# Kernel tuning notes

Hardware: AMD Instinct MI355X
Metric: run time of the kernel (lower is better)

The kernel has to match this reference:

```python
import jax, jax.numpy as jnp
import numpy as np

N = 100000      # nodes
E = 3200000     # edges
F_IN = 512      # input features
H = 16          # hidden dim (as in source)
C = 7           # num classes (Cora)


def gcn_conv(x, W, b, src, dst, n):
    # GCNConv: linear transform, add self-loops, symmetric normalization,
    # scatter-add aggregation from src -> dst, then bias.
    h = x @ W                                   # [N, out]
    loop = jnp.arange(n)
    src_f = jnp.concatenate([src, loop])        # [E+N] with self-loops
    dst_f = jnp.concatenate([dst, loop])
    deg = jax.ops.segment_sum(jnp.ones_like(dst_f, dtype=h.dtype), dst_f, num_segments=n)
    dinv = jnp.where(deg > 0, jax.lax.rsqrt(deg), jnp.zeros_like(deg))
    norm = dinv[src_f] * dinv[dst_f]            # [E+N]
    msg = h[src_f] * norm[:, None]              # gather + scale
    out = jax.ops.segment_sum(msg, dst_f, num_segments=n)  # scatter-add
    return out + b


def setup_inputs() -> dict:
    key = jax.random.key(0)
    k1, k2, k3, k4 = jax.random.split(key, 4)
    x = jax.random.normal(k1, (N, F_IN), dtype=jnp.float32)
    edge_index = jax.random.randint(k2, (2, E), 0, N, dtype=jnp.int32)
    W1 = jax.random.normal(k3, (F_IN, H), dtype=jnp.float32) / np.sqrt(F_IN)
    b1 = jnp.zeros((H,), dtype=jnp.float32)
    W2 = jax.random.normal(k4, (H, C), dtype=jnp.float32) / np.sqrt(H)
    b2 = jnp.zeros((C,), dtype=jnp.float32)
    return {"x": x, "edge_index": edge_index, "W1": W1, "b1": b1, "W2": W2, "b2": b2}


def reference(x, edge_index, W1, b1, W2, b2):
    src, dst = edge_index[0], edge_index[1]
    h = gcn_conv(x, W1, b1, src, dst, N)
    h = jax.nn.relu(h)
    out = gcn_conv(h, W2, b2, src, dst, N)
    return jax.nn.log_softmax(out, axis=1)
```

## Files before the change

### kernel.cpp

```cpp
#include <hip/hip_runtime.h>
#include <math.h>

#define F_IN 512
#define HDIM 16
#define CDIM 7
#define NBLK 1024
#define BSH  9
#define BMASK ((1u << BSH) - 1u)

__global__ __launch_bounds__(256) void k_p2a(const int* __restrict__ dst,
                                             unsigned* __restrict__ hist_g,
                                             int E, int nbuck) {
    __shared__ unsigned lh[256];
    int blk = blockIdx.x;
    int t = threadIdx.x;
    lh[t] = 0u;
    __syncthreads();
    int per = (E + NBLK - 1) / NBLK;
    int s0 = blk * per;
    int e0 = min(E, s0 + per);
    for (int i = s0 + t; i < e0; i += 256)
        atomicAdd(&lh[((unsigned)dst[i]) >> BSH], 1u);
    __syncthreads();
    if (t < nbuck) hist_g[(size_t)t * NBLK + blk] = lh[t];
}

__global__ __launch_bounds__(256) void k_scan_buckets(unsigned* __restrict__ hist_g,
                                                      unsigned* __restrict__ count) {
    __shared__ unsigned s[256];
    int b = blockIdx.x;
    int t = threadIdx.x;
    unsigned* row = hist_g + (size_t)b * NBLK;
    unsigned h[4];
#pragma unroll
    for (int j = 0; j < 4; ++j) h[j] = row[4 * t + j];
    unsigned p = h[0] + h[1] + h[2] + h[3];
    s[t] = p;
    __syncthreads();
    for (int off = 1; off < 256; off <<= 1) {
        unsigned u = (t >= off) ? s[t - off] : 0u;
        __syncthreads();
        s[t] += u;
        __syncthreads();
    }
    unsigned run = s[t] - p;
#pragma unroll
    for (int j = 0; j < 4; ++j) { unsigned hh = h[j]; row[4 * t + j] = run; run += hh; }
    if (t == 255) count[b] = run;
}

__global__ __launch_bounds__(256) void k_scan_tot(const unsigned* __restrict__ count,
                                                  unsigned* __restrict__ boff, int nbuck) {
    __shared__ unsigned s[256];
    int t = threadIdx.x;
    unsigned v = (t < nbuck) ? count[t] : 0u;
    s[t] = v;
    __syncthreads();
    for (int off = 1; off < 256; off <<= 1) {
        unsigned u = (t >= off) ? s[t - off] : 0u;
        __syncthreads();
        s[t] += u;
        __syncthreads();
    }
    if (t < nbuck) boff[t] = s[t] - v;
}

__global__ __launch_bounds__(256) void k_p2b(const int* __restrict__ src,
                                             const int* __restrict__ dst,
                                             const unsigned* __restrict__ hist_g,
                                             const unsigned* __restrict__ boff,
                                             unsigned* __restrict__ pairs,
                                             int E, int nbuck) {
    __shared__ unsigned basel[256];
    __shared__ unsigned cnt[256];
    int blk = blockIdx.x;
    int t = threadIdx.x;
    if (t < nbuck) basel[t] = hist_g[(size_t)t * NBLK + blk] + boff[t];
    cnt[t] = 0u;
    __syncthreads();
    int per = (E + NBLK - 1) / NBLK;
    int s0 = blk * per;
    int e0 = min(E, s0 + per);
    for (int i = s0 + t; i < e0; i += 256) {
        unsigned ss = (unsigned)src[i];
        unsigned dd = (unsigned)dst[i];
        unsigned b = dd >> BSH;
        unsigned r = atomicAdd(&cnt[b], 1u);
        pairs[basel[b] + r] = (ss << BSH) | (dd & BMASK);
    }
}

__global__ __launch_bounds__(1024) void k_p3(const unsigned* __restrict__ pairs,
                                             const unsigned* __restrict__ boff,
                                             const unsigned* __restrict__ count,
                                             unsigned* __restrict__ csr,
                                             unsigned* __restrict__ ptr_g,
                                             unsigned* __restrict__ deg_g,
                                             float* __restrict__ dinv, int n) {
    __shared__ unsigned hist[512];
    __shared__ unsigned cur[512];
    __shared__ unsigned sc[256];
    int b = blockIdx.x;
    int t = threadIdx.x;
    unsigned start = boff[b];
    unsigned cnt = count[b];
    if (t < 512) hist[t] = 0u;
    __syncthreads();
    for (unsigned i = t; i < cnt; i += 1024)
        atomicAdd(&hist[pairs[start + i] & BMASK], 1u);
    __syncthreads();
    unsigned h0 = 0, h1 = 0, part = 0;
    if (t < 256) { h0 = hist[2 * t]; h1 = hist[2 * t + 1]; part = h0 + h1; sc[t] = part; }
    __syncthreads();
    for (int off = 1; off < 256; off <<= 1) {
        unsigned u = 0;
        if (t < 256 && t >= off) u = sc[t - off];
        __syncthreads();
        if (t < 256) sc[t] += u;
        __syncthreads();
    }
    if (t < 256) {
        unsigned x = sc[t] - part;
        cur[2 * t] = x;
        cur[2 * t + 1] = x + h0;
        int base_node = b << BSH;
#pragma unroll
        for (int j = 0; j < 2; ++j) {
            int l = 2 * t + j;
            int node = base_node + l;
            if (node < n) {
                unsigned hv = (j == 0) ? h0 : h1;
                ptr_g[node] = start + cur[l];
                deg_g[node] = hv;
                dinv[node] = rsqrtf((float)hv + 1.0f);
            }
        }
    }
    __syncthreads();
    for (unsigned i = t; i < cnt; i += 1024) {
        unsigned pv = pairs[start + i];
        unsigned slot = atomicAdd(&cur[pv & BMASK], 1u);
        csr[start + slot] = pv >> BSH;
    }
}

__global__ __launch_bounds__(256) void k_gemm1(const float* __restrict__ x,
                                               const float* __restrict__ W,
                                               const float* __restrict__ dinv,
                                               float* __restrict__ g1, int n) {
    int row = blockIdx.x * 256 + threadIdx.x;
    if (row >= n) return;
    const float4* __restrict__ x4 = (const float4*)(x + (size_t)row * F_IN);
    float acc[HDIM];
#pragma unroll
    for (int k = 0; k < HDIM; ++k) acc[k] = 0.f;
#pragma unroll 2
    for (int f4 = 0; f4 < F_IN / 4; ++f4) {
        float4 xv = x4[f4];
#pragma unroll
        for (int j = 0; j < 4; ++j) {
            float xs = (&xv.x)[j];
            const float* wrow = W + (size_t)(f4 * 4 + j) * HDIM;
#pragma unroll
            for (int k = 0; k < HDIM; ++k) acc[k] += xs * wrow[k];
        }
    }
    float di = dinv[row];
    float4* g1o = (float4*)(g1 + (size_t)row * HDIM);
#pragma unroll
    for (int k4 = 0; k4 < 4; ++k4) {
        float4 g;
        g.x = acc[k4 * 4 + 0] * di;
        g.y = acc[k4 * 4 + 1] * di;
        g.z = acc[k4 * 4 + 2] * di;
        g.w = acc[k4 * 4 + 3] * di;
        g1o[k4] = g;
    }
}

__global__ __launch_bounds__(256) void k_gather1(const unsigned* __restrict__ ptr,
                                                 const unsigned* __restrict__ deg,
                                                 const unsigned* __restrict__ csr,
                                                 const float* __restrict__ g1,
                                                 const float* __restrict__ dinv,
                                                 float* __restrict__ agg1, int n) {
    int node = blockIdx.x * 4 + (threadIdx.x >> 6);
    if (node >= n) return;
    int lane = threadIdx.x & 63;
    int k = lane & 15;
    int sub = lane >> 4;
    float acc = (sub == 0) ? g1[(size_t)node * HDIM + k] : 0.f;
    unsigned start = ptr[node];
    unsigned d = deg[node];
    for (unsigned i = sub; i < d; i += 4)
        acc += g1[(size_t)csr[start + i] * HDIM + k];
    acc += __shfl_xor(acc, 16, 64);
    acc += __shfl_xor(acc, 32, 64);
    if (lane < 16) agg1[(size_t)node * HDIM + lane] = acc * dinv[node];
}

__global__ __launch_bounds__(256) void k_layer2(const float* __restrict__ agg1,
                                                const float* __restrict__ b1,
                                                const float* __restrict__ W2,
                                                const float* __restrict__ dinv,
                                                float* __restrict__ g2, int n) {
    int i = blockIdx.x * 256 + threadIdx.x;
    if (i >= n) return;
    float v[HDIM];
    const float4* a4 = (const float4*)(agg1 + (size_t)i * HDIM);
#pragma unroll
    for (int k4 = 0; k4 < 4; ++k4) {
        float4 t = a4[k4];
        v[k4 * 4 + 0] = fmaxf(t.x + b1[k4 * 4 + 0], 0.f);
        v[k4 * 4 + 1] = fmaxf(t.y + b1[k4 * 4 + 1], 0.f);
        v[k4 * 4 + 2] = fmaxf(t.z + b1[k4 * 4 + 2], 0.f);
        v[k4 * 4 + 3] = fmaxf(t.w + b1[k4 * 4 + 3], 0.f);
    }
    float di = dinv[i];
#pragma unroll
    for (int c = 0; c < CDIM; ++c) {
        float h = 0.f;
#pragma unroll
        for (int k = 0; k < HDIM; ++k) h += v[k] * W2[(size_t)k * CDIM + c];
        g2[(size_t)i * 8 + c] = h * di;
    }
    g2[(size_t)i * 8 + 7] = 0.f;
}

__global__ __launch_bounds__(256) void k_gather2_out(const unsigned* __restrict__ ptr,
                                                     const unsigned* __restrict__ deg,
                                                     const unsigned* __restrict__ csr,
                                                     const float* __restrict__ g2,
                                                     const float* __restrict__ dinv,
                                                     const float* __restrict__ b2,
                                                     float* __restrict__ out, int n) {
    int node = blockIdx.x * 4 + (threadIdx.x >> 6);
    if (node >= n) return;
    int lane = threadIdx.x & 63;
    int k = lane & 7;
    int sub = lane >> 3;
    float acc = (sub == 0) ? g2[(size_t)node * 8 + k] : 0.f;
    unsigned start = ptr[node];
    unsigned d = deg[node];
    for (unsigned i = sub; i < d; i += 8)
        acc += g2[(size_t)csr[start + i] * 8 + k];
    acc += __shfl_xor(acc, 8, 64);
    acc += __shfl_xor(acc, 16, 64);
    acc += __shfl_xor(acc, 32, 64);
    float z = (k < CDIM) ? acc * dinv[node] + b2[k] : -1e30f;
    float m = z;
    m = fmaxf(m, __shfl_xor(m, 1, 64));
    m = fmaxf(m, __shfl_xor(m, 2, 64));
    m = fmaxf(m, __shfl_xor(m, 4, 64));
    float ex = (k < CDIM) ? expf(z - m) : 0.f;
    float ssum = ex;
    ssum += __shfl_xor(ssum, 1, 64);
    ssum += __shfl_xor(ssum, 2, 64);
    ssum += __shfl_xor(ssum, 4, 64);
    if (lane < CDIM) out[(size_t)node * CDIM + lane] = z - m - logf(ssum);
}

static inline size_t align4w(size_t w) { return (w + 3) & ~(size_t)3; }

extern "C" void kernel_launch(void* const* d_in, const int* in_sizes, int n_in,
                              void* d_out, int out_size, void* d_ws, size_t ws_size,
                              hipStream_t stream) {
    const float* x  = (const float*)d_in[0];
    const int*   ei = (const int*)d_in[1];
    const float* W1 = (const float*)d_in[2];
    const float* b1 = (const float*)d_in[3];
    const float* W2 = (const float*)d_in[4];
    const float* b2 = (const float*)d_in[5];
    float* out = (float*)d_out;

    int n = in_sizes[0] / F_IN;
    int E = in_sizes[1] / 2;
    const int* src = ei;
    const int* dst = ei + E;
    int nbuck = (n + (1 << BSH) - 1) >> BSH;

    int nb = (n + 255) / 256;
    int gb = (n + 3) / 4;

    unsigned* w = (unsigned*)d_ws;
    size_t o = 0;
    unsigned* hist_g = w + o;             o += align4w((size_t)nbuck * NBLK);
    unsigned* count  = w + o;             o += align4w((size_t)nbuck);
    unsigned* boff   = w + o;             o += align4w((size_t)nbuck);
    unsigned* pairs  = w + o;             o += align4w((size_t)E);
    unsigned* csr    = w + o;             o += align4w((size_t)E);
    unsigned* ptr    = w + o;             o += align4w((size_t)n);
    unsigned* deg    = w + o;             o += align4w((size_t)n);
    float*    dinv   = (float*)(w + o);   o += align4w((size_t)n);
    float*    g1     = (float*)(w + o);   o += align4w((size_t)n * HDIM);
    float*    agg1   = (float*)(w + o);   o += align4w((size_t)n * HDIM);
    float*    g2     = (float*)(w + o);   o += align4w((size_t)n * 8);

    hipLaunchKernelGGL(k_p2a,          dim3(NBLK),  dim3(256),  0, stream, dst, hist_g, E, nbuck);
    hipLaunchKernelGGL(k_scan_buckets, dim3(nbuck), dim3(256),  0, stream, hist_g, count);
    hipLaunchKernelGGL(k_scan_tot,     dim3(1),     dim3(256),  0, stream, count, boff, nbuck);
    hipLaunchKernelGGL(k_p2b,          dim3(NBLK),  dim3(256),  0, stream, src, dst, hist_g, boff, pairs, E, nbuck);
    hipLaunchKernelGGL(k_p3,           dim3(nbuck), dim3(1024), 0, stream, pairs, boff, count, csr, ptr, deg, dinv, n);
    hipLaunchKernelGGL(k_gemm1,        dim3(nb),    dim3(256),  0, stream, x, W1, dinv, g1, n);
    hipLaunchKernelGGL(k_gather1,      dim3(gb),    dim3(256),  0, stream, ptr, deg, csr, g1, dinv, agg1, n);
    hipLaunchKernelGGL(k_layer2,       dim3(nb),    dim3(256),  0, stream, agg1, b1, W2, dinv, g2, n);
    hipLaunchKernelGGL(k_gather2_out,  dim3(gb),    dim3(256),  0, stream, ptr, deg, csr, g2, dinv, b2, out, n);
}
```

Baseline: 560.1 us.

## Replace CSR build with bucket-local shared-memory atomic aggregation

```diff
diff --git a/kernel.cpp b/kernel.cpp
--- a/kernel.cpp
+++ b/kernel.cpp
@@ -5,13 +5,14 @@
 #define HDIM 16
 #define CDIM 7
 #define NBLK 1024
-#define BSH  9
+#define BSH  8
+#define NPB  (1 << BSH)
 #define BMASK ((1u << BSH) - 1u)
 
-__global__ __launch_bounds__(256) void k_p2a(const int* __restrict__ dst,
+__global__ __launch_bounds__(512) void k_p2a(const int* __restrict__ dst,
                                              unsigned* __restrict__ hist_g,
                                              int E, int nbuck) {
-    __shared__ unsigned lh[256];
+    __shared__ unsigned lh[512];
     int blk = blockIdx.x;
     int t = threadIdx.x;
     lh[t] = 0u;
@@ -19,7 +20,7 @@
     int per = (E + NBLK - 1) / NBLK;
     int s0 = blk * per;
     int e0 = min(E, s0 + per);
-    for (int i = s0 + t; i < e0; i += 256)
+    for (int i = s0 + t; i < e0; i += 512)
         atomicAdd(&lh[((unsigned)dst[i]) >> BSH], 1u);
     __syncthreads();
     if (t < nbuck) hist_g[(size_t)t * NBLK + blk] = lh[t];
@@ -49,14 +50,14 @@
     if (t == 255) count[b] = run;
 }
 
-__global__ __launch_bounds__(256) void k_scan_tot(const unsigned* __restrict__ count,
+__global__ __launch_bounds__(512) void k_scan_tot(const unsigned* __restrict__ count,
                                                   unsigned* __restrict__ boff, int nbuck) {
-    __shared__ unsigned s[256];
+    __shared__ unsigned s[512];
     int t = threadIdx.x;
     unsigned v = (t < nbuck) ? count[t] : 0u;
     s[t] = v;
     __syncthreads();
-    for (int off = 1; off < 256; off <<= 1) {
+    for (int off = 1; off < 512; off <<= 1) {
         unsigned u = (t >= off) ? s[t - off] : 0u;
         __syncthreads();
         s[t] += u;
@@ -71,12 +72,14 @@
                                              const unsigned* __restrict__ boff,
                                              unsigned* __restrict__ pairs,
                                              int E, int nbuck) {
-    __shared__ unsigned basel[256];
-    __shared__ unsigned cnt[256];
+    __shared__ unsigned basel[512];
+    __shared__ unsigned cnt[512];
     int blk = blockIdx.x;
     int t = threadIdx.x;
-    if (t < nbuck) basel[t] = hist_g[(size_t)t * NBLK + blk] + boff[t];
-    cnt[t] = 0u;
+    for (int i = t; i < nbuck; i += 256) {
+        basel[i] = hist_g[(size_t)i * NBLK + blk] + boff[i];
+        cnt[i] = 0u;
+    }
     __syncthreads();
     int per = (E + NBLK - 1) / NBLK;
     int s0 = blk * per;
@@ -90,57 +93,23 @@
     }
 }
 
-__global__ __launch_bounds__(1024) void k_p3(const unsigned* __restrict__ pairs,
+__global__ __launch_bounds__(512) void k_deg(const unsigned* __restrict__ pairs,
                                              const unsigned* __restrict__ boff,
                                              const unsigned* __restrict__ count,
-                                             unsigned* __restrict__ csr,
-                                             unsigned* __restrict__ ptr_g,
-                                             unsigned* __restrict__ deg_g,
                                              float* __restrict__ dinv, int n) {
-    __shared__ unsigned hist[512];
-    __shared__ unsigned cur[512];
-    __shared__ unsigned sc[256];
+    __shared__ unsigned h[NPB];
     int b = blockIdx.x;
     int t = threadIdx.x;
+    if (t < NPB) h[t] = 0u;
+    __syncthreads();
     unsigned start = boff[b];
     unsigned cnt = count[b];
-    if (t < 512) hist[t] = 0u;
-    __syncthreads();
-    for (unsigned i = t; i < cnt; i += 1024)
-        atomicAdd(&hist[pairs[start + i] & BMASK], 1u);
-    __syncthreads();
-    unsigned h0 = 0, h1 = 0, part = 0;
-    if (t < 256) { h0 = hist[2 * t]; h1 = hist[2 * t + 1]; part = h0 + h1; sc[t] = part; }
-    __syncthreads();
-    for (int off = 1; off < 256; off <<= 1) {
-        unsigned u = 0;
-        if (t < 256 && t >= off) u = sc[t - off];
-        __syncthreads();
-        if (t < 256) sc[t] += u;
-        __syncthreads();
-    }
-    if (t < 256) {
-        unsigned x = sc[t] - part;
-        cur[2 * t] = x;
-        cur[2 * t + 1] = x + h0;
-        int base_node = b << BSH;
-#pragma unroll
-        for (int j = 0; j < 2; ++j) {
-            int l = 2 * t + j;
-            int node = base_node + l;
-            if (node < n) {
-                unsigned hv = (j == 0) ? h0 : h1;
-                ptr_g[node] = start + cur[l];
-                deg_g[node] = hv;
-                dinv[node] = rsqrtf((float)hv + 1.0f);
-            }
-        }
-    }
-    __syncthreads();
-    for (unsigned i = t; i < cnt; i += 1024) {
-        unsigned pv = pairs[start + i];
-        unsigned slot = atomicAdd(&cur[pv & BMASK], 1u);
-        csr[start + slot] = pv >> BSH;
+    for (unsigned i = t; i < cnt; i += 512)
+        atomicAdd(&h[pairs[start + i] & BMASK], 1u);
+    __syncthreads();
+    if (t < NPB) {
+        int node = (b << BSH) + t;
+        if (node < n) dinv[node] = rsqrtf((float)h[t] + 1.0f);
     }
 }
 
@@ -178,25 +147,42 @@
     }
 }
 
-__global__ __launch_bounds__(256) void k_gather1(const unsigned* __restrict__ ptr,
-                                                 const unsigned* __restrict__ deg,
-                                                 const unsigned* __restrict__ csr,
-                                                 const float* __restrict__ g1,
-                                                 const float* __restrict__ dinv,
-                                                 float* __restrict__ agg1, int n) {
-    int node = blockIdx.x * 4 + (threadIdx.x >> 6);
-    if (node >= n) return;
-    int lane = threadIdx.x & 63;
-    int k = lane & 15;
-    int sub = lane >> 4;
-    float acc = (sub == 0) ? g1[(size_t)node * HDIM + k] : 0.f;
-    unsigned start = ptr[node];
-    unsigned d = deg[node];
-    for (unsigned i = sub; i < d; i += 4)
-        acc += g1[(size_t)csr[start + i] * HDIM + k];
-    acc += __shfl_xor(acc, 16, 64);
-    acc += __shfl_xor(acc, 32, 64);
-    if (lane < 16) agg1[(size_t)node * HDIM + lane] = acc * dinv[node];
+__global__ __launch_bounds__(512) void k_agg1(const unsigned* __restrict__ pairs,
+                                              const unsigned* __restrict__ boff,
+                                              const unsigned* __restrict__ count,
+                                              const float* __restrict__ g1,
+                                              const float* __restrict__ dinv,
+                                              float* __restrict__ agg1, int n) {
+    __shared__ float acc[NPB * HDIM];
+    int b = blockIdx.x;
+    int t = threadIdx.x;
+    for (int i = t; i < NPB * HDIM; i += 512) acc[i] = 0.f;
+    __syncthreads();
+    unsigned start = boff[b];
+    unsigned cnt = count[b];
+    int k = t & 15;
+    unsigned slot = t >> 4;
+    unsigned i = slot;
+    for (; i + 32 < cnt; i += 64) {
+        unsigned pv0 = pairs[start + i];
+        unsigned pv1 = pairs[start + i + 32];
+        float v0 = g1[(size_t)(pv0 >> BSH) * HDIM + k];
+        float v1 = g1[(size_t)(pv1 >> BSH) * HDIM + k];
+        atomicAdd(&acc[(pv0 & BMASK) * HDIM + k], v0);
+        atomicAdd(&acc[(pv1 & BMASK) * HDIM + k], v1);
+    }
+    if (i < cnt) {
+        unsigned pv = pairs[start + i];
+        atomicAdd(&acc[(pv & BMASK) * HDIM + k], g1[(size_t)(pv >> BSH) * HDIM + k]);
+    }
+    __syncthreads();
+    for (int j = t; j < NPB * HDIM; j += 512) {
+        int l = j >> 4;
+        int node = (b << BSH) + l;
+        if (node < n)
+            agg1[(size_t)node * HDIM + (j & 15)] =
+                (acc[j] + g1[(size_t)node * HDIM + (j & 15)]) * dinv[node];
+    }
 }
 
 __global__ __launch_bounds__(256) void k_layer2(const float* __restrict__ agg1,
@@ -227,37 +213,55 @@
     g2[(size_t)i * 8 + 7] = 0.f;
 }
 
-__global__ __launch_bounds__(256) void k_gather2_out(const unsigned* __restrict__ ptr,
-                                                     const unsigned* __restrict__ deg,
-                                                     const unsigned* __restrict__ csr,
-                                                     const float* __restrict__ g2,
-                                                     const float* __restrict__ dinv,
-                                                     const float* __restrict__ b2,
-                                                     float* __restrict__ out, int n) {
-    int node = blockIdx.x * 4 + (threadIdx.x >> 6);
-    if (node >= n) return;
-    int lane = threadIdx.x & 63;
-    int k = lane & 7;
-    int sub = lane >> 3;
-    float acc = (sub == 0) ? g2[(size_t)node * 8 + k] : 0.f;
-    unsigned start = ptr[node];
-    unsigned d = deg[node];
-    for (unsigned i = sub; i < d; i += 8)
-        acc += g2[(size_t)csr[start + i] * 8 + k];
-    acc += __shfl_xor(acc, 8, 64);
-    acc += __shfl_xor(acc, 16, 64);
-    acc += __shfl_xor(acc, 32, 64);
-    float z = (k < CDIM) ? acc * dinv[node] + b2[k] : -1e30f;
-    float m = z;
-    m = fmaxf(m, __shfl_xor(m, 1, 64));
-    m = fmaxf(m, __shfl_xor(m, 2, 64));
-    m = fmaxf(m, __shfl_xor(m, 4, 64));
-    float ex = (k < CDIM) ? expf(z - m) : 0.f;
-    float ssum = ex;
-    ssum += __shfl_xor(ssum, 1, 64);
-    ssum += __shfl_xor(ssum, 2, 64);
-    ssum += __shfl_xor(ssum, 4, 64);
-    if (lane < CDIM) out[(size_t)node * CDIM + lane] = z - m - logf(ssum);
+__global__ __launch_bounds__(512) void k_agg2_out(const unsigned* __restrict__ pairs,
+                                                  const unsigned* __restrict__ boff,
+                                                  const unsigned* __restrict__ count,
+                                                  const float* __restrict__ g2,
+                                                  const float* __restrict__ dinv,
+                                                  const float* __restrict__ b2,
+                                                  float* __restrict__ out, int n) {
+    __shared__ float acc[NPB * 8];
+    int b = blockIdx.x;
+    int t = threadIdx.x;
+    for (int i = t; i < NPB * 8; i += 512) acc[i] = 0.f;
+    __syncthreads();
+    unsigned start = boff[b];
+    unsigned cnt = count[b];
+    int k = t & 7;
+    unsigned slot = t >> 3;
+    unsigned i = slot;
+    for (; i + 64 < cnt; i += 128) {
+        unsigned pv0 = pairs[start + i];
+        unsigned pv1 = pairs[start + i + 64];
+        float v0 = g2[(size_t)(pv0 >> BSH) * 8 + k];
+        float v1 = g2[(size_t)(pv1 >> BSH) * 8 + k];
+        atomicAdd(&acc[(pv0 & BMASK) * 8 + k], v0);
+        atomicAdd(&acc[(pv1 & BMASK) * 8 + k], v1);
+    }
+    if (i < cnt) {
+        unsigned pv = pairs[start + i];
+        atomicAdd(&acc[(pv & BMASK) * 8 + k], g2[(size_t)(pv >> BSH) * 8 + k]);
+    }
+    __syncthreads();
+    if (t < NPB) {
+        int node = (b << BSH) + t;
+        if (node < n) {
+            float di = dinv[node];
+            float z[CDIM];
+            float m = -1e30f;
+#pragma unroll
+            for (int c = 0; c < CDIM; ++c) {
+                z[c] = (acc[t * 8 + c] + g2[(size_t)node * 8 + c]) * di + b2[c];
+                m = fmaxf(m, z[c]);
+            }
+            float ssum = 0.f;
+#pragma unroll
+            for (int c = 0; c < CDIM; ++c) ssum += expf(z[c] - m);
+            float l = logf(ssum);
+#pragma unroll
+            for (int c = 0; c < CDIM; ++c) out[(size_t)node * CDIM + c] = z[c] - m - l;
+        }
+    }
 }
 
 static inline size_t align4w(size_t w) { return (w + 3) & ~(size_t)3; }
@@ -277,10 +281,9 @@
     int E = in_sizes[1] / 2;
     const int* src = ei;
     const int* dst = ei + E;
-    int nbuck = (n + (1 << BSH) - 1) >> BSH;
+    int nbuck = (n + NPB - 1) >> BSH;
 
     int nb = (n + 255) / 256;
-    int gb = (n + 3) / 4;
 
     unsigned* w = (unsigned*)d_ws;
     size_t o = 0;
@@ -288,21 +291,18 @@
     unsigned* count  = w + o;             o += align4w((size_t)nbuck);
     unsigned* boff   = w + o;             o += align4w((size_t)nbuck);
     unsigned* pairs  = w + o;             o += align4w((size_t)E);
-    unsigned* csr    = w + o;             o += align4w((size_t)E);
-    unsigned* ptr    = w + o;             o += align4w((size_t)n);
-    unsigned* deg    = w + o;             o += align4w((size_t)n);
     float*    dinv   = (float*)(w + o);   o += align4w((size_t)n);
     float*    g1     = (float*)(w + o);   o += align4w((size_t)n * HDIM);
     float*    agg1   = (float*)(w + o);   o += align4w((size_t)n * HDIM);
     float*    g2     = (float*)(w + o);   o += align4w((size_t)n * 8);
 
-    hipLaunchKernelGGL(k_p2a,          dim3(NBLK),  dim3(256),  0, stream, dst, hist_g, E, nbuck);
-    hipLaunchKernelGGL(k_scan_buckets, dim3(nbuck), dim3(256),  0, stream, hist_g, count);
-    hipLaunchKernelGGL(k_scan_tot,     dim3(1),     dim3(256),  0, stream, count, boff, nbuck);
-    hipLaunchKernelGGL(k_p2b,          dim3(NBLK),  dim3(256),  0, stream, src, dst, hist_g, boff, pairs, E, nbuck);
-    hipLaunchKernelGGL(k_p3,           dim3(nbuck), dim3(1024), 0, stream, pairs, boff, count, csr, ptr, deg, dinv, n);
-    hipLaunchKernelGGL(k_gemm1,        dim3(nb),    dim3(256),  0, stream, x, W1, dinv, g1, n);
-    hipLaunchKernelGGL(k_gather1,      dim3(gb),    dim3(256),  0, stream, ptr, deg, csr, g1, dinv, agg1, n);
-    hipLaunchKernelGGL(k_layer2,       dim3(nb),    dim3(256),  0, stream, agg1, b1, W2, dinv, g2, n);
-    hipLaunchKernelGGL(k_gather2_out,  dim3(gb),    dim3(256),  0, stream, ptr, deg, csr, g2, dinv, b2, out, n);
-}
+    hipLaunchKernelGGL(k_p2a,          dim3(NBLK),  dim3(512), 0, stream, dst, hist_g, E, nbuck);
+    hipLaunchKernelGGL(k_scan_buckets, dim3(nbuck), dim3(256), 0, stream, hist_g, count);
+    hipLaunchKernelGGL(k_scan_tot,     dim3(1),     dim3(512), 0, stream, count, boff, nbuck);
+    hipLaunchKernelGGL(k_p2b,          dim3(NBLK),  dim3(256), 0, stream, src, dst, hist_g, boff, pairs, E, nbuck);
+    hipLaunchKernelGGL(k_deg,          dim3(nbuck), dim3(512), 0, stream, pairs, boff, count, dinv, n);
+    hipLaunchKernelGGL(k_gemm1,        dim3(nb),    dim3(256), 0, stream, x, W1, dinv, g1, n);
+    hipLaunchKernelGGL(k_agg1,         dim3(nbuck), dim3(512), 0, stream, pairs, boff, count, g1, dinv, agg1, n);
+    hipLaunchKernelGGL(k_layer2,       dim3(nb),    dim3(256), 0, stream, agg1, b1, W2, dinv, g2, n);
+    hipLaunchKernelGGL(k_agg2_out,     dim3(nbuck), dim3(512), 0, stream, pairs, boff, count, g2, dinv, b2, out, n);
+}
```

After: 915.5 us. 1.63x slower.

## Split GEMM1 K across waves, shrink CSR buckets, unroll gather loops

Applied to the files above, without the earlier changes.

```diff
diff --git a/kernel.cpp b/kernel.cpp
--- a/kernel.cpp
+++ b/kernel.cpp
@@ -5,13 +5,14 @@
 #define HDIM 16
 #define CDIM 7
 #define NBLK 1024
-#define BSH  9
+#define BSH  8
+#define NPB  (1 << BSH)
 #define BMASK ((1u << BSH) - 1u)
 
-__global__ __launch_bounds__(256) void k_p2a(const int* __restrict__ dst,
+__global__ __launch_bounds__(512) void k_p2a(const int* __restrict__ dst,
                                              unsigned* __restrict__ hist_g,
                                              int E, int nbuck) {
-    __shared__ unsigned lh[256];
+    __shared__ unsigned lh[512];
     int blk = blockIdx.x;
     int t = threadIdx.x;
     lh[t] = 0u;
@@ -19,7 +20,7 @@
     int per = (E + NBLK - 1) / NBLK;
     int s0 = blk * per;
     int e0 = min(E, s0 + per);
-    for (int i = s0 + t; i < e0; i += 256)
+    for (int i = s0 + t; i < e0; i += 512)
         atomicAdd(&lh[((unsigned)dst[i]) >> BSH], 1u);
     __syncthreads();
     if (t < nbuck) hist_g[(size_t)t * NBLK + blk] = lh[t];
@@ -49,14 +50,14 @@
     if (t == 255) count[b] = run;
 }
 
-__global__ __launch_bounds__(256) void k_scan_tot(const unsigned* __restrict__ count,
+__global__ __launch_bounds__(512) void k_scan_tot(const unsigned* __restrict__ count,
                                                   unsigned* __restrict__ boff, int nbuck) {
-    __shared__ unsigned s[256];
+    __shared__ unsigned s[512];
     int t = threadIdx.x;
     unsigned v = (t < nbuck) ? count[t] : 0u;
     s[t] = v;
     __syncthreads();
-    for (int off = 1; off < 256; off <<= 1) {
+    for (int off = 1; off < 512; off <<= 1) {
         unsigned u = (t >= off) ? s[t - off] : 0u;
         __syncthreads();
         s[t] += u;
@@ -65,23 +66,25 @@
     if (t < nbuck) boff[t] = s[t] - v;
 }
 
-__global__ __launch_bounds__(256) void k_p2b(const int* __restrict__ src,
+__global__ __launch_bounds__(512) void k_p2b(const int* __restrict__ src,
                                              const int* __restrict__ dst,
                                              const unsigned* __restrict__ hist_g,
                                              const unsigned* __restrict__ boff,
                                              unsigned* __restrict__ pairs,
                                              int E, int nbuck) {
-    __shared__ unsigned basel[256];
-    __shared__ unsigned cnt[256];
+    __shared__ unsigned basel[512];
+    __shared__ unsigned cnt[512];
     int blk = blockIdx.x;
     int t = threadIdx.x;
-    if (t < nbuck) basel[t] = hist_g[(size_t)t * NBLK + blk] + boff[t];
-    cnt[t] = 0u;
+    for (int i = t; i < nbuck; i += 512) {
+        basel[i] = hist_g[(size_t)i * NBLK + blk] + boff[i];
+        cnt[i] = 0u;
+    }
     __syncthreads();
     int per = (E + NBLK - 1) / NBLK;
     int s0 = blk * per;
     int e0 = min(E, s0 + per);
-    for (int i = s0 + t; i < e0; i += 256) {
+    for (int i = s0 + t; i < e0; i += 512) {
         unsigned ss = (unsigned)src[i];
         unsigned dd = (unsigned)dst[i];
         unsigned b = dd >> BSH;
@@ -97,43 +100,36 @@
                                              unsigned* __restrict__ ptr_g,
                                              unsigned* __restrict__ deg_g,
                                              float* __restrict__ dinv, int n) {
-    __shared__ unsigned hist[512];
-    __shared__ unsigned cur[512];
-    __shared__ unsigned sc[256];
+    __shared__ unsigned hist[NPB];
+    __shared__ unsigned cur[NPB];
+    __shared__ unsigned sc[NPB];
     int b = blockIdx.x;
     int t = threadIdx.x;
     unsigned start = boff[b];
     unsigned cnt = count[b];
-    if (t < 512) hist[t] = 0u;
+    if (t < NPB) hist[t] = 0u;
     __syncthreads();
     for (unsigned i = t; i < cnt; i += 1024)
         atomicAdd(&hist[pairs[start + i] & BMASK], 1u);
     __syncthreads();
-    unsigned h0 = 0, h1 = 0, part = 0;
-    if (t < 256) { h0 = hist[2 * t]; h1 = hist[2 * t + 1]; part = h0 + h1; sc[t] = part; }
-    __syncthreads();
-    for (int off = 1; off < 256; off <<= 1) {
+    unsigned part = 0;
+    if (t < NPB) { part = hist[t]; sc[t] = part; }
+    __syncthreads();
+    for (int off = 1; off < NPB; off <<= 1) {
         unsigned u = 0;
-        if (t < 256 && t >= off) u = sc[t - off];
-        __syncthreads();
-        if (t < 256) sc[t] += u;
-        __syncthreads();
-    }
-    if (t < 256) {
+        if (t < NPB && t >= off) u = sc[t - off];
+        __syncthreads();
+        if (t < NPB) sc[t] += u;
+        __syncthreads();
+    }
+    if (t < NPB) {
         unsigned x = sc[t] - part;
-        cur[2 * t] = x;
-        cur[2 * t + 1] = x + h0;
-        int base_node = b << BSH;
-#pragma unroll
-        for (int j = 0; j < 2; ++j) {
-            int l = 2 * t + j;
-            int node = base_node + l;
-            if (node < n) {
-                unsigned hv = (j == 0) ? h0 : h1;
-                ptr_g[node] = start + cur[l];
-                deg_g[node] = hv;
-                dinv[node] = rsqrtf((float)hv + 1.0f);
-            }
+        cur[t] = x;
+        int node = (b << BSH) + t;
+        if (node < n) {
+            ptr_g[node] = start + x;
+            deg_g[node] = part;
+            dinv[node] = rsqrtf((float)part + 1.0f);
         }
     }
     __syncthreads();
@@ -148,33 +144,36 @@
                                                const float* __restrict__ W,
                                                const float* __restrict__ dinv,
                                                float* __restrict__ g1, int n) {
-    int row = blockIdx.x * 256 + threadIdx.x;
-    if (row >= n) return;
-    const float4* __restrict__ x4 = (const float4*)(x + (size_t)row * F_IN);
+    __shared__ float sacc[256 * HDIM];
+    int t = threadIdx.x;
+    int lane = t & 63;
+    int q = __builtin_amdgcn_readfirstlane(t >> 6);
+    int row = blockIdx.x * 64 + lane;
     float acc[HDIM];
 #pragma unroll
     for (int k = 0; k < HDIM; ++k) acc[k] = 0.f;
-#pragma unroll 2
-    for (int f4 = 0; f4 < F_IN / 4; ++f4) {
-        float4 xv = x4[f4];
-#pragma unroll
-        for (int j = 0; j < 4; ++j) {
-            float xs = (&xv.x)[j];
-            const float* wrow = W + (size_t)(f4 * 4 + j) * HDIM;
-#pragma unroll
-            for (int k = 0; k < HDIM; ++k) acc[k] += xs * wrow[k];
+    if (row < n) {
+        const float4* __restrict__ x4 = (const float4*)(x + (size_t)row * F_IN) + q * 32;
+#pragma unroll 4
+        for (int i = 0; i < 32; ++i) {
+            float4 xv = x4[i];
+            const float* wr = W + (size_t)(q * 32 + i) * 4 * HDIM;
+#pragma unroll
+            for (int j = 0; j < 4; ++j) {
+                float xs = (&xv.x)[j];
+#pragma unroll
+                for (int k = 0; k < HDIM; ++k) acc[k] += xs * wr[j * HDIM + k];
+            }
         }
     }
-    float di = dinv[row];
-    float4* g1o = (float4*)(g1 + (size_t)row * HDIM);
-#pragma unroll
-    for (int k4 = 0; k4 < 4; ++k4) {
-        float4 g;
-        g.x = acc[k4 * 4 + 0] * di;
-        g.y = acc[k4 * 4 + 1] * di;
-        g.z = acc[k4 * 4 + 2] * di;
-        g.w = acc[k4 * 4 + 3] * di;
-        g1o[k4] = g;
+    float* sa = sacc + (size_t)t * HDIM;
+#pragma unroll
+    for (int k = 0; k < HDIM; ++k) sa[k] = acc[k];
+    __syncthreads();
+    for (int idx = t; idx < 64 * HDIM; idx += 256) {
+        float s = sacc[idx] + sacc[64 * HDIM + idx] + sacc[128 * HDIM + idx] + sacc[192 * HDIM + idx];
+        int node = blockIdx.x * 64 + (idx >> 4);
+        if (node < n) g1[(size_t)node * HDIM + (idx & 15)] = s * dinv[node];
     }
 }
 
@@ -189,11 +188,20 @@
     int lane = threadIdx.x & 63;
     int k = lane & 15;
     int sub = lane >> 4;
-    float acc = (sub == 0) ? g1[(size_t)node * HDIM + k] : 0.f;
+    float acc0 = (sub == 0) ? g1[(size_t)node * HDIM + k] : 0.f;
+    float acc1 = 0.f;
     unsigned start = ptr[node];
     unsigned d = deg[node];
-    for (unsigned i = sub; i < d; i += 4)
-        acc += g1[(size_t)csr[start + i] * HDIM + k];
+    unsigned i = sub;
+    for (; i + 4 < d; i += 8) {
+        unsigned s0 = csr[start + i];
+        unsigned s1 = csr[start + i + 4];
+        acc0 += g1[(size_t)s0 * HDIM + k];
+        acc1 += g1[(size_t)s1 * HDIM + k];
+    }
+    for (; i < d; i += 4)
+        acc0 += g1[(size_t)csr[start + i] * HDIM + k];
+    float acc = acc0 + acc1;
     acc += __shfl_xor(acc, 16, 64);
     acc += __shfl_xor(acc, 32, 64);
     if (lane < 16) agg1[(size_t)node * HDIM + lane] = acc * dinv[node];
@@ -239,11 +247,20 @@
     int lane = threadIdx.x & 63;
     int k = lane & 7;
     int sub = lane >> 3;
-    float acc = (sub == 0) ? g2[(size_t)node * 8 + k] : 0.f;
+    float acc0 = (sub == 0) ? g2[(size_t)node * 8 + k] : 0.f;
+    float acc1 = 0.f;
     unsigned start = ptr[node];
     unsigned d = deg[node];
-    for (unsigned i = sub; i < d; i += 8)
-        acc += g2[(size_t)csr[start + i] * 8 + k];
+    unsigned i = sub;
+    for (; i + 8 < d; i += 16) {
+        unsigned s0 = csr[start + i];
+        unsigned s1 = csr[start + i + 8];
+        acc0 += g2[(size_t)s0 * 8 + k];
+        acc1 += g2[(size_t)s1 * 8 + k];
+    }
+    for (; i < d; i += 8)
+        acc0 += g2[(size_t)csr[start + i] * 8 + k];
+    float acc = acc0 + acc1;
     acc += __shfl_xor(acc, 8, 64);
     acc += __shfl_xor(acc, 16, 64);
     acc += __shfl_xor(acc, 32, 64);
@@ -277,9 +294,10 @@
     int E = in_sizes[1] / 2;
     const int* src = ei;
     const int* dst = ei + E;
-    int nbuck = (n + (1 << BSH) - 1) >> BSH;
+    int nbuck = (n + NPB - 1) >> BSH;
 
     int nb = (n + 255) / 256;
+    int gemb = (n + 63) / 64;
     int gb = (n + 3) / 4;
 
     unsigned* w = (unsigned*)d_ws;
@@ -296,12 +314,12 @@
     float*    agg1   = (float*)(w + o);   o += align4w((size_t)n * HDIM);
     float*    g2     = (float*)(w + o);   o += align4w((size_t)n * 8);
 
-    hipLaunchKernelGGL(k_p2a,          dim3(NBLK),  dim3(256),  0, stream, dst, hist_g, E, nbuck);
+    hipLaunchKernelGGL(k_p2a,          dim3(NBLK),  dim3(512),  0, stream, dst, hist_g, E, nbuck);
     hipLaunchKernelGGL(k_scan_buckets, dim3(nbuck), dim3(256),  0, stream, hist_g, count);
-    hipLaunchKernelGGL(k_scan_tot,     dim3(1),     dim3(256),  0, stream, count, boff, nbuck);
-    hipLaunchKernelGGL(k_p2b,          dim3(NBLK),  dim3(256),  0, stream, src, dst, hist_g, boff, pairs, E, nbuck);
+    hipLaunchKernelGGL(k_scan_tot,     dim3(1),     dim3(512),  0, stream, count, boff, nbuck);
+    hipLaunchKernelGGL(k_p2b,          dim3(NBLK),  dim3(512),  0, stream, src, dst, hist_g, boff, pairs, E, nbuck);
     hipLaunchKernelGGL(k_p3,           dim3(nbuck), dim3(1024), 0, stream, pairs, boff, count, csr, ptr, deg, dinv, n);
-    hipLaunchKernelGGL(k_gemm1,        dim3(nb),    dim3(256),  0, stream, x, W1, dinv, g1, n);
+    hipLaunchKernelGGL(k_gemm1,        dim3(gemb),  dim3(256),  0, stream, x, W1, dinv, g1, n);
     hipLaunchKernelGGL(k_gather1,      dim3(gb),    dim3(256),  0, stream, ptr, deg, csr, g1, dinv, agg1, n);
     hipLaunchKernelGGL(k_layer2,       dim3(nb),    dim3(256),  0, stream, agg1, b1, W2, dinv, g2, n);
     hipLaunchKernelGGL(k_gather2_out,  dim3(gb),    dim3(256),  0, stream, ptr, deg, csr, g2, dinv, b2, out, n);
```

New measurement: 512.1 us. -8.6%, faster.
